# Performance work log

Hardware: AMD Instinct MI355X
Metric: run time of the kernel (lower is better)

Reference implementation:

```python
import jax, jax.numpy as jnp
import numpy as np

V, E, H, L, B, T = 20000, 128, 192, 3, 256, 512


def _lstm_dir(x, W_ih, W_hh, b, reverse):
    """One direction of one LSTM layer. x: [B,T,I] -> (outputs [B,T,H], final h [B,H]).
    PyTorch gate order: i, f, g, o. b = b_ih + b_hh (summed, same math)."""
    gx = jnp.einsum('bti,gi->tbg', x, W_ih) + b  # [T,B,4H] input contributions, precomputed
    Wh = W_hh.T                                   # [H,4H]

    def step(carry, g):
        h, c = carry
        z = g + h @ Wh                            # [B,4H]
        i, f, gg, o = jnp.split(z, 4, axis=-1)
        c = jax.nn.sigmoid(f) * c + jax.nn.sigmoid(i) * jnp.tanh(gg)
        h = jax.nn.sigmoid(o) * jnp.tanh(c)
        return (h, c), h

    h0 = jnp.zeros((x.shape[0], H), x.dtype)
    (hT, _), hs = jax.lax.scan(step, (h0, h0), gx, reverse=reverse)
    return hs.transpose(1, 0, 2), hT


def setup_inputs() -> dict:
    key = jax.random.key(0)
    ks = jax.random.split(key, 12)
    k = 1.0 / np.sqrt(H)
    u = lambda kk, shape: jax.random.uniform(kk, shape, jnp.float32, -k, k)
    emb = jax.random.normal(ks[0], (V, E), jnp.float32)
    emb = emb.at[0].set(0.0)  # padding_idx=0
    return {
        'x': jax.random.randint(ks[1], (B, T), 0, V),
        'emb': emb,
        'W_ih0': u(ks[2], (2, 4 * H, E)),        # layer 0, [dir, 4H, E]
        'W_hh0': u(ks[3], (2, 4 * H, H)),
        'b0': u(ks[4], (2, 4 * H)) + u(ks[5], (2, 4 * H)),  # b_ih + b_hh
        'W_ih_r': u(ks[6], (L - 1, 2, 4 * H, 2 * H)),       # layers 1..2 take concat(fwd,bwd)
        'W_hh_r': u(ks[7], (L - 1, 2, 4 * H, H)),
        'b_r': u(ks[8], (L - 1, 2, 4 * H)) + u(ks[9], (L - 1, 2, 4 * H)),
        'fc_w': u(ks[10], (1, 2 * H)),
        'fc_b': u(ks[11], (1,)),
    }


def reference(x, emb, W_ih0, W_hh0, b0, W_ih_r, W_hh_r, b_r, fc_w, fc_b):
    h = emb[x]  # [B,T,E]
    hT_f = hT_b = None
    for l in range(L):
        if l == 0:
            Wi, Wh, bb = W_ih0, W_hh0, b0
        else:
            Wi, Wh, bb = W_ih_r[l - 1], W_hh_r[l - 1], b_r[l - 1]
        out_f, hT_f = _lstm_dir(h, Wi[0], Wh[0], bb[0], reverse=False)
        out_b, hT_b = _lstm_dir(h, Wi[1], Wh[1], bb[1], reverse=True)
        h = jnp.concatenate([out_f, out_b], axis=-1)  # [B,T,2H]
        # inter-layer dropout is inactive at inference
    last = jnp.concatenate([hT_f, hT_b], axis=-1)     # [B,2H]  (hidden[-2], hidden[-1])
    return last @ fc_w.T + fc_b                        # [B,1]
```

## Files before the change

### kernel.cpp

```cpp
#include <hip/hip_runtime.h>
#include <hip/hip_bf16.h>


typedef _Float16 f16;
typedef unsigned int u32;
typedef _Float16 f16x8 __attribute__((ext_vector_type(8)));
typedef float f32x4 __attribute__((ext_vector_type(4)));

__device__ __forceinline__ float sigm(float x) {
  float e = __builtin_amdgcn_exp2f(x * -1.44269504088896f);
  return __builtin_amdgcn_rcpf(1.0f + e);
}
__device__ __forceinline__ float tanh_(float x) {
  float e = __builtin_amdgcn_exp2f(x * -2.88539008177793f);
  return __builtin_fmaf(2.0f, __builtin_amdgcn_rcpf(1.0f + e), -1.0f);
}


__global__ void castk(const float* __restrict__ s, f16* __restrict__ d, int n) {
  int i = blockIdx.x * 256 + threadIdx.x;
  int st = gridDim.x * 256;
  for (; i < n; i += st) d[i] = (f16)s[i];
}

__global__ void castwhh(const float* __restrict__ src, f16* __restrict__ dst) {
  int o = blockIdx.x * 256 + threadIdx.x;
  int e = o & 7, rest = o >> 3;
  int l = rest & 63; rest >>= 6;
  int kk = rest % 6; rest /= 6;
  int g = rest & 3; rest >>= 2;
  int w = rest % 12; int dir = rest / 12;
  int lo16 = l & 15, lhi = l >> 4;
  dst[o] = (f16)src[(size_t)(dir * 768 + g * 192 + w * 16 + lo16) * 192 + kk * 32 + lhi * 8 + e];
}

__global__ void embedk(const int* __restrict__ x, const float* __restrict__ emb,
                       f16* __restrict__ A0) {
  int row = blockIdx.x * 8 + (threadIdx.x >> 5);
  int t = row >> 8, b = row & 255;
  int xi = x[b * 512 + t];
  int c = (threadIdx.x & 31) * 4;
  float4 v = *(const float4*)(emb + (size_t)xi * 128 + c);
  union { f16 h[4]; uint2 u; } p;
  p.h[0] = (f16)v.x; p.h[1] = (f16)v.y; p.h[2] = (f16)v.z; p.h[3] = (f16)v.w;
  *(uint2*)(A0 + (size_t)row * 128 + c) = p.u;
}

template <int KD>
__global__ __launch_bounds__(768)
void fusedk(const f16* __restrict__ in, const f16* __restrict__ Bt,
            const float* __restrict__ bias,
            const u32* __restrict__ gxR, u32* __restrict__ gxW,
            const f16* __restrict__ whh16,
            f16* __restrict__ outh, float* __restrict__ hT,
            f16* __restrict__ carh, float* __restrict__ carc,
            int c, int cg, int NC, int TC, int doLstm, int wOut, int wHT) {
  union SMem {
    struct { uint4 A[512]; uint4 B[1536]; } g;
    f16 hb[2][16 * 200];
  };
  __shared__ __align__(16) SMem sm;
  const int wg = blockIdx.x;
  const int tid = threadIdx.x;
  const int l = tid & 63, w = tid >> 6;
  const int lo16 = l & 15, lhi = l >> 4;
  const int TCm1 = TC - 1;

  if (doLstm && wg < 32) {
    const int dir = wg & 1, bblk = wg >> 1;
    const int u0 = w * 16;
    const int bb = bblk * 16 + lhi * 4;
    const int dc = dir * 192;
    const int hb0 = lhi * 800 + u0 + lo16;

    f16x8 wf[4][6];
#pragma unroll
    for (int g = 0; g < 4; ++g)
#pragma unroll
      for (int kk = 0; kk < 6; ++kk)
        wf[g][kk] = *(const f16x8*)(whh16 + ((((size_t)dir * 12 + w) * 4 + g) * 6 + kk) * 512 + l * 8);

    float cq[4];
    if (c == 0) {
      f16* hz = (f16*)sm.hb;
      for (int i = tid; i < 2 * 16 * 200; i += 768) hz[i] = (f16)0.f;
#pragma unroll
      for (int q = 0; q < 4; ++q) cq[q] = 0.f;
    } else {
#pragma unroll
      for (int q = 0; q < 4; ++q) {
        size_t ci = ((size_t)dir * 256 + bb + q) * 192 + u0 + lo16;
        cq[q] = carc[ci];
        sm.hb[0][(lhi * 4 + q) * 200 + u0 + lo16] = carh[ci];
      }
    }
    __syncthreads();

    const int tb0 = dir ? (511 - c * TC) : (c * TC);
    f16* outp = outh + ((size_t)tb0 * 256 + bb) * 384 + dc + u0 + lo16;
    const ptrdiff_t ostep = dir ? -(ptrdiff_t)98304 : (ptrdiff_t)98304;

    u32 ga[8], gb[8];
    {
      const int tl0 = dir ? TCm1 : 0;
      size_t wb = ((((size_t)dir * TC + tl0) * 16 + bblk) * 12 + w) * 512;
#pragma unroll
      for (int k2 = 0; k2 < 8; ++k2) ga[k2] = gxR[wb + k2 * 64 + l];
    }

#define RSTEP(S, CUR, NXT)                                                         \
  do {                                                                             \
    {                                                                              \
      int snx = ((S) + 1 < TC) ? (S) + 1 : (S);                                    \
      int tln = dir ? (TCm1 - snx) : snx;                                          \
      size_t wb = ((((size_t)dir * TC + tln) * 16 + bblk) * 12 + w) * 512;         \
      _Pragma("unroll") for (int k2 = 0; k2 < 8; ++k2) NXT[k2] = gxR[wb + k2 * 64 + l]; \
    }                                                                              \
    f32x4 ac[4];                                                                   \
    _Pragma("unroll") for (int g_ = 0; g_ < 4; ++g_) {                             \
      union { u32 u; f16 h[2]; } p0, p1;                                           \
      p0.u = CUR[2 * g_]; p1.u = CUR[2 * g_ + 1];                                  \
      ac[g_][0] = (float)p0.h[0]; ac[g_][1] = (float)p0.h[1];                      \
      ac[g_][2] = (float)p1.h[0]; ac[g_][3] = (float)p1.h[1];                      \
    }                                                                              \
    {                                                                              \
      const f16* hcur = sm.hb[(S) & 1];                                            \
      _Pragma("unroll") for (int kk = 0; kk < 6; ++kk) {                           \
        f16x8 av = *(const f16x8*)(hcur + lo16 * 200 + kk * 32 + lhi * 8);         \
        ac[0] = __builtin_amdgcn_mfma_f32_16x16x32_f16(av, wf[0][kk], ac[0], 0, 0, 0); \
        ac[1] = __builtin_amdgcn_mfma_f32_16x16x32_f16(av, wf[1][kk], ac[1], 0, 0, 0); \
        ac[2] = __builtin_amdgcn_mfma_f32_16x16x32_f16(av, wf[2][kk], ac[2], 0, 0, 0); \
        ac[3] = __builtin_amdgcn_mfma_f32_16x16x32_f16(av, wf[3][kk], ac[3], 0, 0, 0); \
      }                                                                            \
    }                                                                              \
    f16* hnew = sm.hb[((S) + 1) & 1];                                              \
    _Pragma("unroll") for (int q = 0; q < 4; ++q) {                                \
      float iv = sigm(ac[0][q]), fv = sigm(ac[1][q]);                              \
      float gv = tanh_(ac[2][q]), ov = sigm(ac[3][q]);                             \
      cq[q] = fv * cq[q] + iv * gv;                                                \
      float hv = ov * tanh_(cq[q]);                                                \
      f16 hh = (f16)hv;                                                            \
      hnew[hb0 + q * 200] = hh;                                                    \
      if (wOut) outp[q * 384] = hh;                                                \
      if ((S) == TCm1) {                                                           \
        size_t ci = ((size_t)dir * 256 + bb + q) * 192 + u0 + lo16;                \
        carh[ci] = hh;                                                             \
        carc[ci] = cq[q];                                                          \
        if (wHT && c == NC - 1) hT[ci] = hv;                                       \
      }                                                                            \
    }                                                                              \
    outp += ostep;                                                                 \
    asm volatile("s_waitcnt lgkmcnt(0)" ::: "memory");                             \
    __builtin_amdgcn_s_barrier();                                                  \
    asm volatile("" ::: "memory");                                                 \
  } while (0)

    for (int s = 0; s < TC; s += 2) {
      RSTEP(s, ga, gb);
      RSTEP(s + 1, gb, ga);
    }
#undef RSTEP
    return;
  }

  if (cg >= NC) return;
  const int pool = doLstm ? 224 : 256;
  const int gid = doLstm ? wg - 32 : wg;
  const int RT = TC * 4;
  const int ntiles = RT * 8;
  const int tbf = cg * TC, tbb = 512 - (cg + 1) * TC;
  const int wmm = w / 6, wn = w % 6;
  constexpr int NKc = KD / 64;

  for (int tt = gid; tt < ntiles; tt += pool) {
    const int g = tt & 3;
    const int r = (tt >> 2) % RT;
    const int dir = (tt >> 2) / RT;
    const size_t ar0 = (size_t)(dir ? tbb : tbf) * 256 + r * 64;
    const int btr0 = dir * 768 + g * 192;

    float bj[2];
#pragma unroll
    for (int j = 0; j < 2; ++j) bj[j] = bias[btr0 + wn * 32 + j * 16 + lo16];

    f32x4 acc[2][2] = {};
    uint4 a0v, b0v, b1v;

#define LDG(ko_)                                                                   \
  do {                                                                             \
    if (tid < 512) {                                                               \
      int row = tid >> 3, sl = tid & 7, ch = sl ^ (row & 7);                       \
      a0v = *(const uint4*)(in + (ar0 + row) * KD + (ko_)*64 + ch * 8);            \
    }                                                                              \
    { int row = tid >> 3, sl = tid & 7, ch = sl ^ (row & 7);                       \
      b0v = *(const uint4*)(Bt + (size_t)(btr0 + row) * KD + (ko_)*64 + ch * 8); } \
    { int idx = tid + 768; int row = idx >> 3, sl = idx & 7, ch = sl ^ (row & 7);  \
      b1v = *(const uint4*)(Bt + (size_t)(btr0 + row) * KD + (ko_)*64 + ch * 8); } \
  } while (0)

    LDG(0);
    for (int ko = 0; ko < NKc; ++ko) {
      __syncthreads();
      if (tid < 512) sm.g.A[tid] = a0v;
      sm.g.B[tid] = b0v;
      sm.g.B[tid + 768] = b1v;
      __syncthreads();
      if (ko + 1 < NKc) LDG(ko + 1);
#pragma unroll
      for (int kk = 0; kk < 2; ++kk) {
        f16x8 af[2], bf[2];
#pragma unroll
        for (int i = 0; i < 2; ++i) {
          int rowA = wmm * 32 + i * 16 + lo16;
          int slA = (kk * 4 + lhi) ^ (rowA & 7);
          af[i] = *(const f16x8*)((const char*)sm.g.A + rowA * 128 + slA * 16);
        }
#pragma unroll
        for (int j = 0; j < 2; ++j) {
          int colB = wn * 32 + j * 16 + lo16;
          int slB = (kk * 4 + lhi) ^ (colB & 7);
          bf[j] = *(const f16x8*)((const char*)sm.g.B + colB * 128 + slB * 16);
        }
#pragma unroll
        for (int i = 0; i < 2; ++i)
#pragma unroll
          for (int j = 0; j < 2; ++j)
            acc[i][j] = __builtin_amdgcn_mfma_f32_16x16x32_f16(af[i], bf[j], acc[i][j], 0, 0, 0);
      }
    }
#undef LDG

#pragma unroll
    for (int i = 0; i < 2; ++i) {
      int rl = r * 64 + wmm * 32 + i * 16 + lhi * 4;
      int tl = rl >> 8;
      int b16 = (rl & 255) >> 4;
#pragma unroll
      for (int j = 0; j < 2; ++j) {
        int w12 = wn * 2 + j;
        size_t base = ((((size_t)dir * TC + tl) * 16 + b16) * 12 + w12) * 512;
#pragma unroll
        for (int qq = 0; qq < 2; ++qq) {
          union { f16 h[2]; u32 u; } p;
          p.h[0] = (f16)(acc[i][j][2 * qq] + bj[j]);
          p.h[1] = (f16)(acc[i][j][2 * qq + 1] + bj[j]);
          gxW[base + (g * 2 + qq) * 64 + l] = p.u;
        }
      }
    }
    __syncthreads();
  }
}

__global__ void fck(const float* __restrict__ hT, const float* __restrict__ w,
                    const float* __restrict__ fb, float* __restrict__ out) {
  int b = blockIdx.x * 64 + threadIdx.x;
  float a = fb[0];
#pragma unroll 4
  for (int u = 0; u < 192; ++u)
    a += w[u] * hT[(size_t)b * 192 + u] + w[192 + u] * hT[49152 + (size_t)b * 192 + u];
  out[b] = a;
}

extern "C" void kernel_launch(void* const* d_in, const int* in_sizes, int n_in,
                              void* d_out, int out_size, void* d_ws, size_t ws_size,
                              hipStream_t stream) {
  (void)in_sizes; (void)n_in; (void)out_size;
  const int* x = (const int*)d_in[0];
  const float* emb = (const float*)d_in[1];
  const float* Wih0 = (const float*)d_in[2];
  const float* Whh0 = (const float*)d_in[3];
  const float* b0 = (const float*)d_in[4];
  const float* Wihr = (const float*)d_in[5];
  const float* Whhr = (const float*)d_in[6];
  const float* br = (const float*)d_in[7];
  const float* fcw = (const float*)d_in[8];
  const float* fcb = (const float*)d_in[9];
  float* out = (float*)d_out;

  const size_t hB = 100663296ull;
  const size_t fixedB = 2 * hB + 1179648ull + 589824ull + 393216ull + 196608ull + 393216ull;

  int TC = (ws_size >= fixedB + 2ull * 16 * 786432ull) ? 16 : 8;
  const int NC = 512 / TC;
  const size_t chunkB = (size_t)TC * 786432ull;

  char* ws = (char*)d_ws;
  u32* gxb[2] = {(u32*)ws, (u32*)(ws + chunkB)};
  size_t off = 2 * chunkB;
  f16* h0 = (f16*)(ws + off); off += hB;
  f16* h1 = (f16*)(ws + off); off += hB;
  f16* A0 = h1;
  f16* Bt = (f16*)(ws + off); off += 1179648ull;
  f16* whh16 = (f16*)(ws + off); off += 589824ull;
  float* hT = (float*)(ws + off); off += 393216ull;
  f16* carh = (f16*)(ws + off); off += 196608ull;
  float* carc = (float*)(ws + off); off += 393216ull;

  embedk<<<16384, 256, 0, stream>>>(x, emb, A0);

  for (int layer = 0; layer < 3; ++layer) {
    const f16* in = (layer == 0) ? A0 : (layer == 1 ? h0 : h1);
    f16* outp = (layer == 1) ? h1 : h0;
    const int wOut = (layer < 2) ? 1 : 0;
    const int wHT = (layer == 2) ? 1 : 0;
    const float* bias = (layer == 0) ? b0 : (br + (layer - 1) * 1536);

    if (layer == 0) {
      castk<<<192, 256, 0, stream>>>(Wih0, Bt, 196608);
      castwhh<<<1152, 256, 0, stream>>>(Whh0, whh16);
    } else {
      castk<<<1152, 256, 0, stream>>>(Wihr + (size_t)(layer - 1) * 589824, Bt, 589824);
      castwhh<<<1152, 256, 0, stream>>>(Whhr + (size_t)(layer - 1) * 294912, whh16);
    }

    if (layer == 0)
      fusedk<128><<<256, 768, 0, stream>>>(in, Bt, bias, gxb[0], gxb[0], whh16,
                                           outp, hT, carh, carc, 0, 0, NC, TC, 0, wOut, wHT);
    else
      fusedk<384><<<256, 768, 0, stream>>>(in, Bt, bias, gxb[0], gxb[0], whh16,
                                           outp, hT, carh, carc, 0, 0, NC, TC, 0, wOut, wHT);

    for (int c = 0; c < NC; ++c) {
      const u32* gR = gxb[c & 1];
      u32* gW = gxb[(c + 1) & 1];
      if (layer == 0)
        fusedk<128><<<256, 768, 0, stream>>>(in, Bt, bias, gR, gW, whh16,
                                             outp, hT, carh, carc, c, c + 1, NC, TC, 1, wOut, wHT);
      else
        fusedk<384><<<256, 768, 0, stream>>>(in, Bt, bias, gR, gW, whh16,
                                             outp, hT, carh, carc, c, c + 1, NC, TC, 1, wOut, wHT);
    }
  }

  fck<<<4, 64, 0, stream>>>(hT, fcw, fcb, out);
}
```

Measured before the change: 2.779 ms.

## Vectorize gx loads/stores, merge cast kernels, and fuse LSTM gate math

Several independent changes. The precomputed gate-input buffer is re-laid out so each lane's 8 words are contiguous, which turns eight strided u32 loads per step into two 16-byte loads and makes the producer write one 8-byte store per tile. The two weight-cast kernels are merged into one launch per layer. The gate nonlinearities are rewritten to share reciprocals (sigmoid*tanh folded into one rcp), with clamped exponents for safety. The shared reciprocals trade a few extra multiplies for fewer rcp instructions on the serial recurrent path and add minor rounding differences.

```diff
diff --git a/kernel.cpp b/kernel.cpp
--- a/kernel.cpp
+++ b/kernel.cpp
@@ -7,31 +7,23 @@
 typedef _Float16 f16x8 __attribute__((ext_vector_type(8)));
 typedef float f32x4 __attribute__((ext_vector_type(4)));
 
-__device__ __forceinline__ float sigm(float x) {
-  float e = __builtin_amdgcn_exp2f(x * -1.44269504088896f);
-  return __builtin_amdgcn_rcpf(1.0f + e);
-}
-__device__ __forceinline__ float tanh_(float x) {
-  float e = __builtin_amdgcn_exp2f(x * -2.88539008177793f);
-  return __builtin_fmaf(2.0f, __builtin_amdgcn_rcpf(1.0f + e), -1.0f);
-}
-
-
-__global__ void castk(const float* __restrict__ s, f16* __restrict__ d, int n) {
+typedef union { uint4 v[2]; u32 d[8]; } gx8;
+
+
+__global__ void castboth(const float* __restrict__ wih, f16* __restrict__ bt, int nbt,
+                         const float* __restrict__ whh, f16* __restrict__ w16) {
   int i = blockIdx.x * 256 + threadIdx.x;
-  int st = gridDim.x * 256;
-  for (; i < n; i += st) d[i] = (f16)s[i];
-}
-
-__global__ void castwhh(const float* __restrict__ src, f16* __restrict__ dst) {
-  int o = blockIdx.x * 256 + threadIdx.x;
-  int e = o & 7, rest = o >> 3;
-  int l = rest & 63; rest >>= 6;
-  int kk = rest % 6; rest /= 6;
-  int g = rest & 3; rest >>= 2;
-  int w = rest % 12; int dir = rest / 12;
-  int lo16 = l & 15, lhi = l >> 4;
-  dst[o] = (f16)src[(size_t)(dir * 768 + g * 192 + w * 16 + lo16) * 192 + kk * 32 + lhi * 8 + e];
+  if (i < nbt) bt[i] = (f16)wih[i];
+  int o = i - nbt;
+  if (o >= 0 && o < 294912) {
+    int e = o & 7, rest = o >> 3;
+    int l = rest & 63; rest >>= 6;
+    int kk = rest % 6; rest /= 6;
+    int g = rest & 3; rest >>= 2;
+    int w = rest % 12; int dir = rest / 12;
+    int lo16 = l & 15, lhi = l >> 4;
+    w16[o] = (f16)whh[(size_t)(dir * 768 + g * 192 + w * 16 + lo16) * 192 + kk * 32 + lhi * 8 + e];
+  }
 }
 
 __global__ void embedk(const int* __restrict__ x, const float* __restrict__ emb,
@@ -99,27 +91,24 @@
     const int tb0 = dir ? (511 - c * TC) : (c * TC);
     f16* outp = outh + ((size_t)tb0 * 256 + bb) * 384 + dc + u0 + lo16;
     const ptrdiff_t ostep = dir ? -(ptrdiff_t)98304 : (ptrdiff_t)98304;
-
-    u32 ga[8], gb[8];
-    {
-      const int tl0 = dir ? TCm1 : 0;
-      size_t wb = ((((size_t)dir * TC + tl0) * 16 + bblk) * 12 + w) * 512;
-#pragma unroll
-      for (int k2 = 0; k2 < 8; ++k2) ga[k2] = gxR[wb + k2 * 64 + l];
-    }
+    const int tl0 = dir ? TCm1 : 0;
+    const u32* gxp = gxR + ((((size_t)dir * TC + tl0) * 16 + bblk) * 12 + w) * 512 + l * 8;
+    const ptrdiff_t gstep = dir ? -(ptrdiff_t)98304 : (ptrdiff_t)98304;
+
+    gx8 ga, gb;
+    ga.v[0] = *(const uint4*)gxp;
+    ga.v[1] = *(const uint4*)(gxp + 4);
 
 #define RSTEP(S, CUR, NXT)                                                         \
   do {                                                                             \
-    {                                                                              \
-      int snx = ((S) + 1 < TC) ? (S) + 1 : (S);                                    \
-      int tln = dir ? (TCm1 - snx) : snx;                                          \
-      size_t wb = ((((size_t)dir * TC + tln) * 16 + bblk) * 12 + w) * 512;         \
-      _Pragma("unroll") for (int k2 = 0; k2 < 8; ++k2) NXT[k2] = gxR[wb + k2 * 64 + l]; \
-    }                                                                              \
+    const u32* gnx = ((S) + 1 < TC) ? (gxp + gstep) : gxp;                         \
+    NXT.v[0] = *(const uint4*)gnx;                                                 \
+    NXT.v[1] = *(const uint4*)(gnx + 4);                                           \
+    gxp = gnx;                                                                     \
     f32x4 ac[4];                                                                   \
     _Pragma("unroll") for (int g_ = 0; g_ < 4; ++g_) {                             \
       union { u32 u; f16 h[2]; } p0, p1;                                           \
-      p0.u = CUR[2 * g_]; p1.u = CUR[2 * g_ + 1];                                  \
+      p0.u = CUR.d[2 * g_]; p1.u = CUR.d[2 * g_ + 1];                              \
       ac[g_][0] = (float)p0.h[0]; ac[g_][1] = (float)p0.h[1];                      \
       ac[g_][2] = (float)p1.h[0]; ac[g_][3] = (float)p1.h[1];                      \
     }                                                                              \
@@ -135,10 +124,15 @@
     }                                                                              \
     f16* hnew = sm.hb[((S) + 1) & 1];                                              \
     _Pragma("unroll") for (int q = 0; q < 4; ++q) {                                \
-      float iv = sigm(ac[0][q]), fv = sigm(ac[1][q]);                              \
-      float gv = tanh_(ac[2][q]), ov = sigm(ac[3][q]);                             \
-      cq[q] = fv * cq[q] + iv * gv;                                                \
-      float hv = ov * tanh_(cq[q]);                                                \
+      float ei = __builtin_amdgcn_exp2f(fminf(ac[0][q] * -1.44269504f, 80.f));     \
+      float ef = __builtin_amdgcn_exp2f(fminf(ac[1][q] * -1.44269504f, 80.f));     \
+      float eg = __builtin_amdgcn_exp2f(fminf(ac[2][q] * -2.88539008f, 80.f));     \
+      float eo = __builtin_amdgcn_exp2f(fminf(ac[3][q] * -1.44269504f, 80.f));     \
+      float ig = (1.f - eg) * __builtin_amdgcn_rcpf((1.f + eg) * (1.f + ei));      \
+      float fv = __builtin_amdgcn_rcpf(1.f + ef);                                  \
+      cq[q] = fv * cq[q] + ig;                                                     \
+      float ec = __builtin_amdgcn_exp2f(fminf(cq[q] * -2.88539008f, 80.f));        \
+      float hv = (1.f - ec) * __builtin_amdgcn_rcpf((1.f + ec) * (1.f + eo));      \
       f16 hh = (f16)hv;                                                            \
       hnew[hb0 + q * 200] = hh;                                                    \
       if (wOut) outp[q * 384] = hh;                                                \
@@ -238,14 +232,14 @@
 #pragma unroll
       for (int j = 0; j < 2; ++j) {
         int w12 = wn * 2 + j;
-        size_t base = ((((size_t)dir * TC + tl) * 16 + b16) * 12 + w12) * 512;
-#pragma unroll
-        for (int qq = 0; qq < 2; ++qq) {
-          union { f16 h[2]; u32 u; } p;
-          p.h[0] = (f16)(acc[i][j][2 * qq] + bj[j]);
-          p.h[1] = (f16)(acc[i][j][2 * qq + 1] + bj[j]);
-          gxW[base + (g * 2 + qq) * 64 + l] = p.u;
-        }
+        size_t seg = ((size_t)(dir * TC + tl) * 16 + b16) * 12 + w12;
+        union { f16 h[2]; u32 u; } q0, q1;
+        q0.h[0] = (f16)(acc[i][j][0] + bj[j]);
+        q0.h[1] = (f16)(acc[i][j][1] + bj[j]);
+        q1.h[0] = (f16)(acc[i][j][2] + bj[j]);
+        q1.h[1] = (f16)(acc[i][j][3] + bj[j]);
+        uint2 pk; pk.x = q0.u; pk.y = q1.u;
+        *(uint2*)(gxW + seg * 512 + l * 8 + g * 2) = pk;
       }
     }
     __syncthreads();
@@ -306,13 +300,12 @@
     const int wHT = (layer == 2) ? 1 : 0;
     const float* bias = (layer == 0) ? b0 : (br + (layer - 1) * 1536);
 
-    if (layer == 0) {
-      castk<<<192, 256, 0, stream>>>(Wih0, Bt, 196608);
-      castwhh<<<1152, 256, 0, stream>>>(Whh0, whh16);
-    } else {
-      castk<<<1152, 256, 0, stream>>>(Wihr + (size_t)(layer - 1) * 589824, Bt, 589824);
-      castwhh<<<1152, 256, 0, stream>>>(Whhr + (size_t)(layer - 1) * 294912, whh16);
-    }
+    if (layer == 0)
+      castboth<<<(196608 + 294912 + 255) / 256, 256, 0, stream>>>(Wih0, Bt, 196608, Whh0, whh16);
+    else
+      castboth<<<(589824 + 294912 + 255) / 256, 256, 0, stream>>>(
+          Wihr + (size_t)(layer - 1) * 589824, Bt, 589824,
+          Whhr + (size_t)(layer - 1) * 294912, whh16);
 
     if (layer == 0)
       fusedk<128><<<256, 768, 0, stream>>>(in, Bt, bias, gxb[0], gxb[0], whh16,
```

Result: slower. 2.918 ms (+5.0%).
